# Kernel tuning notes

Hardware: AMD Instinct MI355X
Metric: run time of the kernel (lower is better)

## Reference

```python
import jax, jax.numpy as jnp
import numpy as np

B, S, D, H = 4, 2048, 1024, 16
HD = D // H  # head_size = 64


def setup_inputs() -> dict:
    key = jax.random.key(0)
    kx, kq, kk, kv = jax.random.split(key, 4)
    scale = 1.0 / np.sqrt(D)
    return {
        "x": jax.random.normal(kx, (B, S, D), dtype=jnp.float32),
        "Wq": jax.random.normal(kq, (H, HD, D), dtype=jnp.float32) * scale,
        "Wk": jax.random.normal(kk, (H, HD, D), dtype=jnp.float32) * scale,
        "Wv": jax.random.normal(kv, (H, HD, D), dtype=jnp.float32) * scale,
    }


def reference(x, Wq, Wk, Wv):
    # Per-head projections (Linear with weight [out, in]: y = x @ W.T),
    # vectorized over heads: [B,S,D] x [H,HD,D] -> [B,H,S,HD]
    q = jnp.einsum('bsd,hed->bhse', x, Wq)
    k = jnp.einsum('bsd,hed->bhse', x, Wk)
    v = jnp.einsum('bsd,hed->bhse', x, Wv)

    # Scaled scores: [B,H,S,S]
    att = jnp.einsum('bhqe,bhke->bhqk', q, k) / jnp.sqrt(jnp.asarray(HD, x.dtype))

    # Causal mask (lower-triangular incl. diagonal)
    causal = jnp.tril(jnp.ones((S, S), dtype=bool))
    att = jnp.where(causal, att, -jnp.inf)
    att = jax.nn.softmax(att, axis=-1)

    # Weighted values, then concat heads along feature dim -> [B,S,D]
    out = jnp.einsum('bhqk,bhke->bhqe', att, v)
    out = out.transpose(0, 2, 1, 3).reshape(B, S, H * HD)
    return out
```

## Files before the change

kernel.cpp:

```cpp
#include <hip/hip_runtime.h>
#include <hip/hip_bf16.h>

#define BATCH 4
#define S_LEN 2048
#define D_DIM 1024
#define NHEAD 16
#define HDIM 64

#define QSCALE 0.18033688011112042f

typedef __attribute__((ext_vector_type(8))) __bf16 bf16x8;
typedef __attribute__((ext_vector_type(4))) __bf16 bf16x4;
typedef __attribute__((ext_vector_type(4))) float f32x4;

static __device__ inline unsigned int bf16_bits(float f) {
    __bf16 h = (__bf16)f;
    return (unsigned int)__builtin_bit_cast(unsigned short, h);
}

__global__ __launch_bounds__(256) void cvt_kernel(
    const float* __restrict__ src, __bf16* __restrict__ dst, int n8)
{
    int i = blockIdx.x * 256 + threadIdx.x;
    if (i >= n8) return;
    const f32x4* p = reinterpret_cast<const f32x4*>(src + (size_t)i * 8);
    f32x4 a = p[0], b = p[1];
    bf16x8 r;
    r[0] = (__bf16)a[0]; r[1] = (__bf16)a[1]; r[2] = (__bf16)a[2]; r[3] = (__bf16)a[3];
    r[4] = (__bf16)b[0]; r[5] = (__bf16)b[1]; r[6] = (__bf16)b[2]; r[7] = (__bf16)b[3];
    *reinterpret_cast<bf16x8*>(dst + (size_t)i * 8) = r;
}

__global__ __launch_bounds__(256) void proj_gemm_kernel(
    const __bf16* __restrict__ xb, const __bf16* __restrict__ wb,
    __bf16* __restrict__ qo, __bf16* __restrict__ ko, __bf16* __restrict__ vto)
{
    __shared__ __bf16 As[128][32];
    __shared__ __bf16 Bs[128][32];

    const int tid = threadIdx.x;
    const int l  = tid & 63;
    const int w  = tid >> 6;
    const int wm = w >> 1, wn = w & 1;
    const int lr = l & 15, lg = l >> 4, lk = lg * 8;
    const int m0 = blockIdx.y * 128;
    const int n0 = blockIdx.x * 128;
    const int mat = n0 >> 10;
    const int nb  = n0 & 1023;

    const int sr = l >> 2;
    const int sc = (l & 3) * 8;
    const int g0 = w * 2;

    f32x4 acc[4][4] = {};

    for (int d = 0; d < D_DIM; d += 32) {
        __builtin_amdgcn_global_load_lds(
            (const __attribute__((address_space(1))) void*)(xb + (size_t)(m0 + g0 * 16 + sr) * D_DIM + d + sc),
            (__attribute__((address_space(3))) void*)(&As[g0 * 16][0]), 16, 0, 0);
        __builtin_amdgcn_global_load_lds(
            (const __attribute__((address_space(1))) void*)(xb + (size_t)(m0 + (g0 + 1) * 16 + sr) * D_DIM + d + sc),
            (__attribute__((address_space(3))) void*)(&As[(g0 + 1) * 16][0]), 16, 0, 0);
        __builtin_amdgcn_global_load_lds(
            (const __attribute__((address_space(1))) void*)(wb + (size_t)(n0 + g0 * 16 + sr) * D_DIM + d + sc),
            (__attribute__((address_space(3))) void*)(&Bs[g0 * 16][0]), 16, 0, 0);
        __builtin_amdgcn_global_load_lds(
            (const __attribute__((address_space(1))) void*)(wb + (size_t)(n0 + (g0 + 1) * 16 + sr) * D_DIM + d + sc),
            (__attribute__((address_space(3))) void*)(&Bs[(g0 + 1) * 16][0]), 16, 0, 0);
        __syncthreads();

        bf16x8 af[4], bfr[4];
        #pragma unroll
        for (int mi = 0; mi < 4; ++mi)
            af[mi] = *reinterpret_cast<const bf16x8*>(&As[wm * 64 + mi * 16 + lr][lk]);
        #pragma unroll
        for (int ni = 0; ni < 4; ++ni)
            bfr[ni] = *reinterpret_cast<const bf16x8*>(&Bs[wn * 64 + ni * 16 + lr][lk]);
        #pragma unroll
        for (int mi = 0; mi < 4; ++mi) {
            #pragma unroll
            for (int ni = 0; ni < 4; ++ni)
                acc[mi][ni] = __builtin_amdgcn_mfma_f32_16x16x32_bf16(
                    af[mi], bfr[ni], acc[mi][ni], 0, 0, 0);
        }
        __syncthreads();
    }

    const float oscale = (mat == 0) ? QSCALE : 1.0f;
    #pragma unroll
    for (int mi = 0; mi < 4; ++mi) {
        const int mrow = m0 + wm * 64 + mi * 16 + lg * 4;
        const int b = mrow >> 11;
        const int s = mrow & (S_LEN - 1);
        #pragma unroll
        for (int ni = 0; ni < 4; ++ni) {
            const int n = nb + wn * 64 + ni * 16 + lr;
            const int h = n >> 6;
            const int e = n & 63;
            if (mat == 2) {
                bf16x4 pk;
                #pragma unroll
                for (int r = 0; r < 4; ++r) pk[r] = (__bf16)acc[mi][ni][r];
                *reinterpret_cast<bf16x4*>(
                    vto + ((size_t)(b * NHEAD + h) * HDIM + e) * S_LEN + s) = pk;
            } else {
                __bf16* __restrict__ dst = (mat == 0) ? qo : ko;
                #pragma unroll
                for (int r = 0; r < 4; ++r)
                    dst[((size_t)(b * NHEAD + h) * S_LEN + (s + r)) * HDIM + e] =
                        (__bf16)(acc[mi][ni][r] * oscale);
            }
        }
    }
}

template<bool MASK>
__device__ __attribute__((always_inline)) inline void quad_iter(
    int kv0, int qbase, int lr, int lg, int lk, int swz,
    const __bf16* __restrict__ kp, const __bf16* __restrict__ vp,
    const bf16x8 (&bq0)[4], const bf16x8 (&bq1)[4],
    float (&m_acc)[4], float (&l_acc)[4], f32x4 (&acc)[4][4],
    __bf16* pl_base)
{
    bf16x8 ka0[4], ka1[4];
    #pragma unroll
    for (int c = 0; c < 4; ++c) {
        const __bf16* krow = kp + (size_t)(kv0 + c * 16 + lr) * HDIM;
        ka0[c] = *reinterpret_cast<const bf16x8*>(krow + lk);
        ka1[c] = *reinterpret_cast<const bf16x8*>(krow + 32 + lk);
    }
    bf16x8 av[2][4];
    #pragma unroll
    for (int c2 = 0; c2 < 2; ++c2)
        #pragma unroll
        for (int ni = 0; ni < 4; ++ni)
            av[c2][ni] = *reinterpret_cast<const bf16x8*>(
                vp + (size_t)(ni * 16 + lr) * S_LEN + kv0 + c2 * 32 + lk);

    #pragma unroll
    for (int i = 0; i < 4; ++i) {
        __bf16* pl = pl_base + i * (16 * 64);
        f32x4 s[4];
        __builtin_amdgcn_s_setprio(1);
        #pragma unroll
        for (int c = 0; c < 4; ++c) {
            f32x4 tt = {};
            tt = __builtin_amdgcn_mfma_f32_16x16x32_bf16(ka0[c], bq0[i], tt, 0, 0, 0);
            tt = __builtin_amdgcn_mfma_f32_16x16x32_bf16(ka1[c], bq1[i], tt, 0, 0, 0);
            s[c] = tt;
        }
        __builtin_amdgcn_s_setprio(0);

        if (MASK) {
            const int qrow = qbase + i * 16 + lr;
            #pragma unroll
            for (int c = 0; c < 4; ++c)
                #pragma unroll
                for (int r = 0; r < 4; ++r)
                    if (kv0 + c * 16 + lg * 4 + r > qrow) s[c][r] = -1e30f;
        }

        float a0 = fmaxf(fmaxf(s[0][0], s[0][1]), fmaxf(s[0][2], s[0][3]));
        float a1 = fmaxf(fmaxf(s[1][0], s[1][1]), fmaxf(s[1][2], s[1][3]));
        float a2 = fmaxf(fmaxf(s[2][0], s[2][1]), fmaxf(s[2][2], s[2][3]));
        float a3 = fmaxf(fmaxf(s[3][0], s[3][1]), fmaxf(s[3][2], s[3][3]));
        float mx = fmaxf(fmaxf(a0, a1), fmaxf(a2, a3));
        mx = fmaxf(mx, __shfl_xor(mx, 16));
        mx = fmaxf(mx, __shfl_xor(mx, 32));

        const float mnew = fmaxf(m_acc[i], mx);
        const float sc = exp2f(m_acc[i] - mnew);
        m_acc[i] = mnew;

        float psum = 0.0f;
        #pragma unroll
        for (int c = 0; c < 4; ++c) {
            const float p0 = exp2f(s[c][0] - mnew);
            const float p1 = exp2f(s[c][1] - mnew);
            const float p2 = exp2f(s[c][2] - mnew);
            const float p3 = exp2f(s[c][3] - mnew);
            psum += (p0 + p1) + (p2 + p3);
            uint2 pk;
            pk.x = bf16_bits(p0) | (bf16_bits(p1) << 16);
            pk.y = bf16_bits(p2) | (bf16_bits(p3) << 16);
            *reinterpret_cast<uint2*>(pl + lr * 64 + ((c * 16 + lg * 4) ^ swz)) = pk;
        }
        psum += __shfl_xor(psum, 16);
        psum += __shfl_xor(psum, 32);
        l_acc[i] = l_acc[i] * sc + psum;

        #pragma unroll
        for (int ni = 0; ni < 4; ++ni) acc[i][ni] *= sc;
    }

    __builtin_amdgcn_s_setprio(1);
    #pragma unroll
    for (int c2 = 0; c2 < 2; ++c2) {
        #pragma unroll
        for (int i = 0; i < 4; ++i) {
            __bf16* pl = pl_base + i * (16 * 64);
            const bf16x8 pa = *reinterpret_cast<const bf16x8*>(
                pl + lr * 64 + ((c2 * 32 + lk) ^ swz));
            #pragma unroll
            for (int ni = 0; ni < 4; ++ni)
                acc[i][ni] = __builtin_amdgcn_mfma_f32_16x16x32_bf16(
                    av[c2][ni], pa, acc[i][ni], 0, 0, 0);
        }
    }
    __builtin_amdgcn_s_setprio(0);
}

__global__ __launch_bounds__(64, 2) void attn_kernel(
    const __bf16* __restrict__ q, const __bf16* __restrict__ k,
    const __bf16* __restrict__ vt, float* __restrict__ out)
{
    __shared__ __bf16 plds[4][16][64];

    const int l  = threadIdx.x;
    const int lr = l & 15;
    const int lg = l >> 4;
    const int lk = lg * 8;
    const int swz = (lr & 7) << 3;

    const int n   = blockIdx.x;
    const int xcd = n & 7;
    const int m   = n >> 3;
    const int qq  = 31 - (m >> 3);
    const int bh  = xcd * 8 + (m & 7);

    const __bf16* __restrict__ kp = k  + (size_t)bh * S_LEN * HDIM;
    const __bf16* __restrict__ vp = vt + (size_t)bh * HDIM * S_LEN;
    const int bq = bh >> 4;
    const int hq = bh & 15;

    const int qbase = qq * 64;
    const int iters = qq + 1;

    const __bf16* __restrict__ qp = q + ((size_t)bh * S_LEN + qbase) * HDIM;
    bf16x8 bq0[4], bq1[4];
    #pragma unroll
    for (int i = 0; i < 4; ++i) {
        bq0[i] = *reinterpret_cast<const bf16x8*>(qp + (size_t)(i * 16 + lr) * HDIM + lk);
        bq1[i] = *reinterpret_cast<const bf16x8*>(qp + (size_t)(i * 16 + lr) * HDIM + 32 + lk);
    }

    float m_acc[4], l_acc[4];
    f32x4 acc[4][4] = {};
    #pragma unroll
    for (int i = 0; i < 4; ++i) { m_acc[i] = -1e30f; l_acc[i] = 0.0f; }

    __bf16* pl_base = &plds[0][0][0];

    #pragma unroll 1
    for (int j = 0; j < iters - 1; ++j)
        quad_iter<false>(j * 64, qbase, lr, lg, lk, swz, kp, vp,
                         bq0, bq1, m_acc, l_acc, acc, pl_base);
    quad_iter<true>((iters - 1) * 64, qbase, lr, lg, lk, swz, kp, vp,
                    bq0, bq1, m_acc, l_acc, acc, pl_base);

    #pragma unroll
    for (int i = 0; i < 4; ++i) {
        const float liv = 1.0f / l_acc[i];
        float* orow = out + (size_t)(bq * S_LEN + qbase + i * 16 + lr) * D_DIM + hq * HDIM;
        #pragma unroll
        for (int ni = 0; ni < 4; ++ni) {
            f32x4 ox;
            #pragma unroll
            for (int r = 0; r < 4; ++r) ox[r] = acc[i][ni][r] * liv;
            *reinterpret_cast<f32x4*>(orow + ni * 16 + lg * 4) = ox;
        }
    }
}

extern "C" void kernel_launch(void* const* d_in, const int* in_sizes, int n_in,
                              void* d_out, int out_size, void* d_ws, size_t ws_size,
                              hipStream_t stream)
{
    const float* x  = (const float*)d_in[0];
    const float* Wq = (const float*)d_in[1];
    const float* Wk = (const float*)d_in[2];
    const float* Wv = (const float*)d_in[3];
    float* out = (float*)d_out;

    const size_t x_elems = (size_t)BATCH * S_LEN * D_DIM;
    const size_t w_elems = (size_t)D_DIM * D_DIM;
    __bf16* xb   = (__bf16*)d_out;
    __bf16* wcat = xb + x_elems;

    const size_t per_buf = (size_t)BATCH * NHEAD * S_LEN * HDIM;
    __bf16* qb = (__bf16*)d_ws;
    __bf16* kb = qb + per_buf;
    __bf16* vb = kb + per_buf;

    cvt_kernel<<<(int)(x_elems / 8 / 256), 256, 0, stream>>>(x, xb, (int)(x_elems / 8));
    cvt_kernel<<<(int)(w_elems / 8 / 256), 256, 0, stream>>>(Wq, wcat, (int)(w_elems / 8));
    cvt_kernel<<<(int)(w_elems / 8 / 256), 256, 0, stream>>>(Wk, wcat + w_elems, (int)(w_elems / 8));
    cvt_kernel<<<(int)(w_elems / 8 / 256), 256, 0, stream>>>(Wv, wcat + 2 * w_elems, (int)(w_elems / 8));

    dim3 grid1(3 * D_DIM / 128, (BATCH * S_LEN) / 128);
    proj_gemm_kernel<<<grid1, dim3(256), 0, stream>>>(xb, wcat, qb, kb, vb);

    attn_kernel<<<dim3(2048), dim3(64), 0, stream>>>(qb, kb, vb, out);
}
```

Baseline: 193.0 us.

## Double-buffer K fragments across KV tiles and interleave softmax of row pairs

Adds register double-buffering of K fragments: the next KV tile's K is prefetched from global memory while the current tile is computed, using two KFrag sets and a ping-pong flag. It also processes two 16-row query sub-blocks at a time so their MFMA chains, reductions and shuffles interleave, and defers the l_acc cross-lane sum until after the PV MFMAs. V loads are reordered so the two halves of each row are fetched together. The extra live registers for the second K buffer raise pressure under launch_bounds(64,2) and may cause spills.

```diff
diff --git a/kernel.cpp b/kernel.cpp
--- a/kernel.cpp
+++ b/kernel.cpp
@@ -114,100 +114,149 @@
     }
 }
 
+struct KFrag { bf16x8 a0[4]; bf16x8 a1[4]; };
+struct VFrag { bf16x8 v0[4]; bf16x8 v1[4]; };
+
+__device__ __attribute__((always_inline)) inline void load_k(
+    KFrag& kf, const __bf16* __restrict__ kp, int kv0, int lr, int lk)
+{
+    #pragma unroll
+    for (int c = 0; c < 4; ++c) {
+        const __bf16* krow = kp + (size_t)(kv0 + c * 16 + lr) * HDIM;
+        kf.a0[c] = *reinterpret_cast<const bf16x8*>(krow + lk);
+        kf.a1[c] = *reinterpret_cast<const bf16x8*>(krow + 32 + lk);
+    }
+}
+
 template<bool MASK>
-__device__ __attribute__((always_inline)) inline void quad_iter(
+__device__ __attribute__((always_inline)) inline void quad_compute(
     int kv0, int qbase, int lr, int lg, int lk, int swz,
-    const __bf16* __restrict__ kp, const __bf16* __restrict__ vp,
+    const __bf16* __restrict__ vp, const KFrag& kf,
     const bf16x8 (&bq0)[4], const bf16x8 (&bq1)[4],
     float (&m_acc)[4], float (&l_acc)[4], f32x4 (&acc)[4][4],
     __bf16* pl_base)
 {
-    bf16x8 ka0[4], ka1[4];
-    #pragma unroll
-    for (int c = 0; c < 4; ++c) {
-        const __bf16* krow = kp + (size_t)(kv0 + c * 16 + lr) * HDIM;
-        ka0[c] = *reinterpret_cast<const bf16x8*>(krow + lk);
-        ka1[c] = *reinterpret_cast<const bf16x8*>(krow + 32 + lk);
-    }
-    bf16x8 av[2][4];
-    #pragma unroll
-    for (int c2 = 0; c2 < 2; ++c2)
-        #pragma unroll
-        for (int ni = 0; ni < 4; ++ni)
-            av[c2][ni] = *reinterpret_cast<const bf16x8*>(
-                vp + (size_t)(ni * 16 + lr) * S_LEN + kv0 + c2 * 32 + lk);
-
-    #pragma unroll
-    for (int i = 0; i < 4; ++i) {
-        __bf16* pl = pl_base + i * (16 * 64);
-        f32x4 s[4];
+    VFrag vf;
+    #pragma unroll
+    for (int ni = 0; ni < 4; ++ni) {
+        const __bf16* vrow = vp + (size_t)(ni * 16 + lr) * S_LEN + kv0;
+        vf.v0[ni] = *reinterpret_cast<const bf16x8*>(vrow + lk);
+        vf.v1[ni] = *reinterpret_cast<const bf16x8*>(vrow + 32 + lk);
+    }
+
+    float sc_t[4], psum_t[4];
+
+    #pragma unroll
+    for (int pp = 0; pp < 2; ++pp) {
+        const int i0 = pp * 2, i1 = pp * 2 + 1;
+        f32x4 sA[4], sB[4];
+
         __builtin_amdgcn_s_setprio(1);
         #pragma unroll
         for (int c = 0; c < 4; ++c) {
-            f32x4 tt = {};
-            tt = __builtin_amdgcn_mfma_f32_16x16x32_bf16(ka0[c], bq0[i], tt, 0, 0, 0);
-            tt = __builtin_amdgcn_mfma_f32_16x16x32_bf16(ka1[c], bq1[i], tt, 0, 0, 0);
-            s[c] = tt;
+            f32x4 t0 = {}, t1 = {};
+            t0 = __builtin_amdgcn_mfma_f32_16x16x32_bf16(kf.a0[c], bq0[i0], t0, 0, 0, 0);
+            t0 = __builtin_amdgcn_mfma_f32_16x16x32_bf16(kf.a1[c], bq1[i0], t0, 0, 0, 0);
+            t1 = __builtin_amdgcn_mfma_f32_16x16x32_bf16(kf.a0[c], bq0[i1], t1, 0, 0, 0);
+            t1 = __builtin_amdgcn_mfma_f32_16x16x32_bf16(kf.a1[c], bq1[i1], t1, 0, 0, 0);
+            sA[c] = t0; sB[c] = t1;
         }
         __builtin_amdgcn_s_setprio(0);
 
         if (MASK) {
-            const int qrow = qbase + i * 16 + lr;
+            const int qrA = qbase + i0 * 16 + lr;
+            const int qrB = qbase + i1 * 16 + lr;
             #pragma unroll
             for (int c = 0; c < 4; ++c)
                 #pragma unroll
-                for (int r = 0; r < 4; ++r)
-                    if (kv0 + c * 16 + lg * 4 + r > qrow) s[c][r] = -1e30f;
-        }
-
-        float a0 = fmaxf(fmaxf(s[0][0], s[0][1]), fmaxf(s[0][2], s[0][3]));
-        float a1 = fmaxf(fmaxf(s[1][0], s[1][1]), fmaxf(s[1][2], s[1][3]));
-        float a2 = fmaxf(fmaxf(s[2][0], s[2][1]), fmaxf(s[2][2], s[2][3]));
-        float a3 = fmaxf(fmaxf(s[3][0], s[3][1]), fmaxf(s[3][2], s[3][3]));
-        float mx = fmaxf(fmaxf(a0, a1), fmaxf(a2, a3));
-        mx = fmaxf(mx, __shfl_xor(mx, 16));
-        mx = fmaxf(mx, __shfl_xor(mx, 32));
-
-        const float mnew = fmaxf(m_acc[i], mx);
-        const float sc = exp2f(m_acc[i] - mnew);
-        m_acc[i] = mnew;
-
-        float psum = 0.0f;
+                for (int r = 0; r < 4; ++r) {
+                    const int kvp = kv0 + c * 16 + lg * 4 + r;
+                    if (kvp > qrA) sA[c][r] = -1e30f;
+                    if (kvp > qrB) sB[c][r] = -1e30f;
+                }
+        }
+
+        float mxA = fmaxf(
+            fmaxf(fmaxf(fmaxf(sA[0][0], sA[0][1]), fmaxf(sA[0][2], sA[0][3])),
+                  fmaxf(fmaxf(sA[1][0], sA[1][1]), fmaxf(sA[1][2], sA[1][3]))),
+            fmaxf(fmaxf(fmaxf(sA[2][0], sA[2][1]), fmaxf(sA[2][2], sA[2][3])),
+                  fmaxf(fmaxf(sA[3][0], sA[3][1]), fmaxf(sA[3][2], sA[3][3]))));
+        float mxB = fmaxf(
+            fmaxf(fmaxf(fmaxf(sB[0][0], sB[0][1]), fmaxf(sB[0][2], sB[0][3])),
+                  fmaxf(fmaxf(sB[1][0], sB[1][1]), fmaxf(sB[1][2], sB[1][3]))),
+            fmaxf(fmaxf(fmaxf(sB[2][0], sB[2][1]), fmaxf(sB[2][2], sB[2][3])),
+                  fmaxf(fmaxf(sB[3][0], sB[3][1]), fmaxf(sB[3][2], sB[3][3]))));
+        float tA = __shfl_xor(mxA, 16);
+        float tB = __shfl_xor(mxB, 16);
+        mxA = fmaxf(mxA, tA);
+        mxB = fmaxf(mxB, tB);
+        tA = __shfl_xor(mxA, 32);
+        tB = __shfl_xor(mxB, 32);
+        mxA = fmaxf(mxA, tA);
+        mxB = fmaxf(mxB, tB);
+
+        const float mnA = fmaxf(m_acc[i0], mxA);
+        const float mnB = fmaxf(m_acc[i1], mxB);
+        sc_t[i0] = exp2f(m_acc[i0] - mnA);
+        sc_t[i1] = exp2f(m_acc[i1] - mnB);
+        m_acc[i0] = mnA;
+        m_acc[i1] = mnB;
+
+        __bf16* plA = pl_base + i0 * (16 * 64);
+        __bf16* plB = pl_base + i1 * (16 * 64);
+        float psA = 0.0f, psB = 0.0f;
         #pragma unroll
         for (int c = 0; c < 4; ++c) {
-            const float p0 = exp2f(s[c][0] - mnew);
-            const float p1 = exp2f(s[c][1] - mnew);
-            const float p2 = exp2f(s[c][2] - mnew);
-            const float p3 = exp2f(s[c][3] - mnew);
-            psum += (p0 + p1) + (p2 + p3);
-            uint2 pk;
-            pk.x = bf16_bits(p0) | (bf16_bits(p1) << 16);
-            pk.y = bf16_bits(p2) | (bf16_bits(p3) << 16);
-            *reinterpret_cast<uint2*>(pl + lr * 64 + ((c * 16 + lg * 4) ^ swz)) = pk;
-        }
-        psum += __shfl_xor(psum, 16);
-        psum += __shfl_xor(psum, 32);
-        l_acc[i] = l_acc[i] * sc + psum;
-
-        #pragma unroll
-        for (int ni = 0; ni < 4; ++ni) acc[i][ni] *= sc;
+            const float a0 = exp2f(sA[c][0] - mnA);
+            const float a1 = exp2f(sA[c][1] - mnA);
+            const float a2 = exp2f(sA[c][2] - mnA);
+            const float a3 = exp2f(sA[c][3] - mnA);
+            const float b0 = exp2f(sB[c][0] - mnB);
+            const float b1 = exp2f(sB[c][1] - mnB);
+            const float b2 = exp2f(sB[c][2] - mnB);
+            const float b3 = exp2f(sB[c][3] - mnB);
+            psA += (a0 + a1) + (a2 + a3);
+            psB += (b0 + b1) + (b2 + b3);
+            uint2 pkA, pkB;
+            pkA.x = bf16_bits(a0) | (bf16_bits(a1) << 16);
+            pkA.y = bf16_bits(a2) | (bf16_bits(a3) << 16);
+            pkB.x = bf16_bits(b0) | (bf16_bits(b1) << 16);
+            pkB.y = bf16_bits(b2) | (bf16_bits(b3) << 16);
+            const int col = (c * 16 + lg * 4) ^ swz;
+            *reinterpret_cast<uint2*>(plA + lr * 64 + col) = pkA;
+            *reinterpret_cast<uint2*>(plB + lr * 64 + col) = pkB;
+        }
+        psum_t[i0] = psA;
+        psum_t[i1] = psB;
+
+        #pragma unroll
+        for (int ni = 0; ni < 4; ++ni) {
+            acc[i0][ni] *= sc_t[i0];
+            acc[i1][ni] *= sc_t[i1];
+        }
     }
 
     __builtin_amdgcn_s_setprio(1);
     #pragma unroll
-    for (int c2 = 0; c2 < 2; ++c2) {
-        #pragma unroll
-        for (int i = 0; i < 4; ++i) {
-            __bf16* pl = pl_base + i * (16 * 64);
-            const bf16x8 pa = *reinterpret_cast<const bf16x8*>(
-                pl + lr * 64 + ((c2 * 32 + lk) ^ swz));
-            #pragma unroll
-            for (int ni = 0; ni < 4; ++ni)
-                acc[i][ni] = __builtin_amdgcn_mfma_f32_16x16x32_bf16(
-                    av[c2][ni], pa, acc[i][ni], 0, 0, 0);
+    for (int i = 0; i < 4; ++i) {
+        __bf16* pl = pl_base + i * (16 * 64);
+        const bf16x8 pa0 = *reinterpret_cast<const bf16x8*>(pl + lr * 64 + ((0 + lk) ^ swz));
+        const bf16x8 pa1 = *reinterpret_cast<const bf16x8*>(pl + lr * 64 + ((32 + lk) ^ swz));
+        #pragma unroll
+        for (int ni = 0; ni < 4; ++ni) {
+            acc[i][ni] = __builtin_amdgcn_mfma_f32_16x16x32_bf16(vf.v0[ni], pa0, acc[i][ni], 0, 0, 0);
+            acc[i][ni] = __builtin_amdgcn_mfma_f32_16x16x32_bf16(vf.v1[ni], pa1, acc[i][ni], 0, 0, 0);
         }
     }
     __builtin_amdgcn_s_setprio(0);
+
+    #pragma unroll
+    for (int i = 0; i < 4; ++i) {
+        float ps = psum_t[i];
+        ps += __shfl_xor(ps, 16);
+        ps += __shfl_xor(ps, 32);
+        l_acc[i] = l_acc[i] * sc_t[i] + ps;
+    }
 }
 
 __global__ __launch_bounds__(64, 2) void attn_kernel(
@@ -251,12 +300,29 @@
 
     __bf16* pl_base = &plds[0][0][0];
 
+    KFrag kA, kB;
+    load_k(kA, kp, 0, lr, lk);
+    bool useA = true;
+
     #pragma unroll 1
-    for (int j = 0; j < iters - 1; ++j)
-        quad_iter<false>(j * 64, qbase, lr, lg, lk, swz, kp, vp,
-                         bq0, bq1, m_acc, l_acc, acc, pl_base);
-    quad_iter<true>((iters - 1) * 64, qbase, lr, lg, lk, swz, kp, vp,
-                    bq0, bq1, m_acc, l_acc, acc, pl_base);
+    for (int j = 0; j < iters - 1; ++j) {
+        if (useA) {
+            load_k(kB, kp, (j + 1) * 64, lr, lk);
+            quad_compute<false>(j * 64, qbase, lr, lg, lk, swz, vp, kA,
+                                bq0, bq1, m_acc, l_acc, acc, pl_base);
+        } else {
+            load_k(kA, kp, (j + 1) * 64, lr, lk);
+            quad_compute<false>(j * 64, qbase, lr, lg, lk, swz, vp, kB,
+                                bq0, bq1, m_acc, l_acc, acc, pl_base);
+        }
+        useA = !useA;
+    }
+    if (useA)
+        quad_compute<true>((iters - 1) * 64, qbase, lr, lg, lk, swz, vp, kA,
+                           bq0, bq1, m_acc, l_acc, acc, pl_base);
+    else
+        quad_compute<true>((iters - 1) * 64, qbase, lr, lg, lk, swz, vp, kB,
+                           bq0, bq1, m_acc, l_acc, acc, pl_base);
 
     #pragma unroll
     for (int i = 0; i < 4; ++i) {
```

Result: slower. 355.8 us (+84.3%).

## Double-buffer K tiles in LDS via async global_load_lds prefetch

Applied to the files above, without the earlier changes.

K tiles now go into a double-buffered LDS region with asynchronous global-to-LDS loads. The next tile is prefetched while the current one is computed, and the K operand is read back from LDS with an XOR swizzle. This is meant to hide global-memory latency for K behind the MFMA and softmax work. The cost is extra LDS use, which can affect occupancy, and manual vmcnt waits. Those waits also count the V global loads, so the vmcnt(8) threshold may not line up with the intended K dependency.

```diff
diff --git a/kernel.cpp b/kernel.cpp
--- a/kernel.cpp
+++ b/kernel.cpp
@@ -114,28 +114,39 @@
     }
 }
 
+__device__ __attribute__((always_inline)) inline void stage_k(
+    __bf16* kbuf, const __bf16* __restrict__ kp, int kv0, int l)
+{
+    const int rsub = l >> 3;
+    const int csw  = ((l & 7) ^ rsub) << 3;
+    #pragma unroll
+    for (int ch = 0; ch < 8; ++ch) {
+        __builtin_amdgcn_global_load_lds(
+            (const __attribute__((address_space(1))) void*)(
+                kp + (size_t)(kv0 + ch * 8 + rsub) * HDIM + csw),
+            (__attribute__((address_space(3))) void*)(kbuf + ch * 512),
+            16, 0, 0);
+    }
+}
+
 template<bool MASK>
-__device__ __attribute__((always_inline)) inline void quad_iter(
+__device__ __attribute__((always_inline)) inline void quad_compute(
     int kv0, int qbase, int lr, int lg, int lk, int swz,
-    const __bf16* __restrict__ kp, const __bf16* __restrict__ vp,
+    const __bf16* __restrict__ vp, const __bf16* __restrict__ kb,
     const bf16x8 (&bq0)[4], const bf16x8 (&bq1)[4],
     float (&m_acc)[4], float (&l_acc)[4], f32x4 (&acc)[4][4],
     __bf16* pl_base)
 {
-    bf16x8 ka0[4], ka1[4];
-    #pragma unroll
-    for (int c = 0; c < 4; ++c) {
-        const __bf16* krow = kp + (size_t)(kv0 + c * 16 + lr) * HDIM;
-        ka0[c] = *reinterpret_cast<const bf16x8*>(krow + lk);
-        ka1[c] = *reinterpret_cast<const bf16x8*>(krow + 32 + lk);
-    }
+    const int kcol0 = (lg * 8) ^ ((lr & 7) << 3);
+    const int kcol1 = (32 + lg * 8) ^ ((lr & 7) << 3);
+
     bf16x8 av[2][4];
     #pragma unroll
-    for (int c2 = 0; c2 < 2; ++c2)
-        #pragma unroll
-        for (int ni = 0; ni < 4; ++ni)
-            av[c2][ni] = *reinterpret_cast<const bf16x8*>(
-                vp + (size_t)(ni * 16 + lr) * S_LEN + kv0 + c2 * 32 + lk);
+    for (int ni = 0; ni < 4; ++ni) {
+        const __bf16* vrow = vp + (size_t)(ni * 16 + lr) * S_LEN + kv0;
+        av[0][ni] = *reinterpret_cast<const bf16x8*>(vrow + lk);
+        av[1][ni] = *reinterpret_cast<const bf16x8*>(vrow + 32 + lk);
+    }
 
     #pragma unroll
     for (int i = 0; i < 4; ++i) {
@@ -144,9 +155,12 @@
         __builtin_amdgcn_s_setprio(1);
         #pragma unroll
         for (int c = 0; c < 4; ++c) {
+            const int row = c * 16 + lr;
+            const bf16x8 ka0 = *reinterpret_cast<const bf16x8*>(kb + row * 64 + kcol0);
+            const bf16x8 ka1 = *reinterpret_cast<const bf16x8*>(kb + row * 64 + kcol1);
             f32x4 tt = {};
-            tt = __builtin_amdgcn_mfma_f32_16x16x32_bf16(ka0[c], bq0[i], tt, 0, 0, 0);
-            tt = __builtin_amdgcn_mfma_f32_16x16x32_bf16(ka1[c], bq1[i], tt, 0, 0, 0);
+            tt = __builtin_amdgcn_mfma_f32_16x16x32_bf16(ka0, bq0[i], tt, 0, 0, 0);
+            tt = __builtin_amdgcn_mfma_f32_16x16x32_bf16(ka1, bq1[i], tt, 0, 0, 0);
             s[c] = tt;
         }
         __builtin_amdgcn_s_setprio(0);
@@ -215,6 +229,7 @@
     const __bf16* __restrict__ vt, float* __restrict__ out)
 {
     __shared__ __bf16 plds[4][16][64];
+    __shared__ __bf16 klds[2][64 * 64];
 
     const int l  = threadIdx.x;
     const int lr = l & 15;
@@ -251,12 +266,25 @@
 
     __bf16* pl_base = &plds[0][0][0];
 
+    stage_k(&klds[0][0], kp, 0, l);
+    asm volatile("s_waitcnt vmcnt(0)" ::: "memory");
+    __builtin_amdgcn_sched_barrier(0);
+
     #pragma unroll 1
-    for (int j = 0; j < iters - 1; ++j)
-        quad_iter<false>(j * 64, qbase, lr, lg, lk, swz, kp, vp,
-                         bq0, bq1, m_acc, l_acc, acc, pl_base);
-    quad_iter<true>((iters - 1) * 64, qbase, lr, lg, lk, swz, kp, vp,
-                    bq0, bq1, m_acc, l_acc, acc, pl_base);
+    for (int j = 0; j < iters - 1; ++j) {
+        stage_k(&klds[(j & 1) ^ 1][0], kp, (j + 1) * 64, l);
+        __builtin_amdgcn_sched_barrier(0);
+        asm volatile("s_waitcnt vmcnt(8)" ::: "memory");
+        __builtin_amdgcn_sched_barrier(0);
+        quad_compute<false>(j * 64, qbase, lr, lg, lk, swz, vp, &klds[j & 1][0],
+                            bq0, bq1, m_acc, l_acc, acc, pl_base);
+    }
+    __builtin_amdgcn_sched_barrier(0);
+    asm volatile("s_waitcnt vmcnt(0)" ::: "memory");
+    __builtin_amdgcn_sched_barrier(0);
+    quad_compute<true>((iters - 1) * 64, qbase, lr, lg, lk, swz, vp,
+                       &klds[(iters - 1) & 1][0],
+                       bq0, bq1, m_acc, l_acc, acc, pl_base);
 
     #pragma unroll
     for (int i = 0; i < 4; ++i) {
```

New measurement: 197.5 us. 2.3% more time.

## Split attention KV loop across two waves and merge partial softmax results

Applied to the files above, without the earlier changes.

Each attention block now runs two wavefronts that take alternating 64-wide KV tiles for the same 64 query rows. Each wave keeps its own running max, sum and accumulator. At the end the partial states are exchanged through shared memory and merged with a rescaled online-softmax combine. The aim is to halve the serial KV loop length per block and improve latency hiding, at the cost of extra LDS traffic, two barriers, and duplicated Q register loads per wave.

```diff
diff --git a/kernel.cpp b/kernel.cpp
--- a/kernel.cpp
+++ b/kernel.cpp
@@ -115,7 +115,7 @@
 }
 
 template<bool MASK>
-__device__ __attribute__((always_inline)) inline void quad_iter(
+__device__ __attribute__((always_inline)) inline void quad_compute(
     int kv0, int qbase, int lr, int lg, int lk, int swz,
     const __bf16* __restrict__ kp, const __bf16* __restrict__ vp,
     const bf16x8 (&bq0)[4], const bf16x8 (&bq1)[4],
@@ -131,11 +131,11 @@
     }
     bf16x8 av[2][4];
     #pragma unroll
-    for (int c2 = 0; c2 < 2; ++c2)
-        #pragma unroll
-        for (int ni = 0; ni < 4; ++ni)
-            av[c2][ni] = *reinterpret_cast<const bf16x8*>(
-                vp + (size_t)(ni * 16 + lr) * S_LEN + kv0 + c2 * 32 + lk);
+    for (int ni = 0; ni < 4; ++ni) {
+        const __bf16* vrow = vp + (size_t)(ni * 16 + lr) * S_LEN + kv0;
+        av[0][ni] = *reinterpret_cast<const bf16x8*>(vrow + lk);
+        av[1][ni] = *reinterpret_cast<const bf16x8*>(vrow + 32 + lk);
+    }
 
     #pragma unroll
     for (int i = 0; i < 4; ++i) {
@@ -210,13 +210,15 @@
     __builtin_amdgcn_s_setprio(0);
 }
 
-__global__ __launch_bounds__(64, 2) void attn_kernel(
+__global__ __launch_bounds__(128, 3) void attn_kernel(
     const __bf16* __restrict__ q, const __bf16* __restrict__ k,
     const __bf16* __restrict__ vt, float* __restrict__ out)
 {
-    __shared__ __bf16 plds[4][16][64];
-
-    const int l  = threadIdx.x;
+    __shared__ __align__(16) unsigned char smem[16384 + 512];
+
+    const int tid = threadIdx.x;
+    const int l  = tid & 63;
+    const int w  = tid >> 6;
     const int lr = l & 15;
     const int lg = l >> 4;
     const int lk = lg * 8;
@@ -234,7 +236,6 @@
     const int hq = bh & 15;
 
     const int qbase = qq * 64;
-    const int iters = qq + 1;
 
     const __bf16* __restrict__ qp = q + ((size_t)bh * S_LEN + qbase) * HDIM;
     bf16x8 bq0[4], bq1[4];
@@ -249,24 +250,53 @@
     #pragma unroll
     for (int i = 0; i < 4; ++i) { m_acc[i] = -1e30f; l_acc[i] = 0.0f; }
 
-    __bf16* pl_base = &plds[0][0][0];
+    __bf16* pl_base = reinterpret_cast<__bf16*>(smem) + w * 4096;
 
     #pragma unroll 1
-    for (int j = 0; j < iters - 1; ++j)
-        quad_iter<false>(j * 64, qbase, lr, lg, lk, swz, kp, vp,
-                         bq0, bq1, m_acc, l_acc, acc, pl_base);
-    quad_iter<true>((iters - 1) * 64, qbase, lr, lg, lk, swz, kp, vp,
-                    bq0, bq1, m_acc, l_acc, acc, pl_base);
-
-    #pragma unroll
-    for (int i = 0; i < 4; ++i) {
-        const float liv = 1.0f / l_acc[i];
-        float* orow = out + (size_t)(bq * S_LEN + qbase + i * 16 + lr) * D_DIM + hq * HDIM;
+    for (int j = w; j < qq; j += 2)
+        quad_compute<false>(j * 64, qbase, lr, lg, lk, swz, kp, vp,
+                            bq0, bq1, m_acc, l_acc, acc, pl_base);
+    if ((qq & 1) == w)
+        quad_compute<true>(qq * 64, qbase, lr, lg, lk, swz, kp, vp,
+                           bq0, bq1, m_acc, l_acc, acc, pl_base);
+
+    float* accbuf = reinterpret_cast<float*>(smem);
+    float* mbuf   = reinterpret_cast<float*>(smem + 16384);
+    float* lbuf   = mbuf + 64;
+
+    __syncthreads();
+    #pragma unroll
+    for (int tt = 0; tt < 2; ++tt) {
+        const int t = 2 * w + tt;
+        #pragma unroll
+        for (int ni = 0; ni < 4; ++ni)
+            #pragma unroll
+            for (int r = 0; r < 4; ++r)
+                accbuf[t * 1024 + (ni * 16 + lg * 4 + r) * 16 + lr] = acc[t][ni][r];
+        if (lg == 0) {
+            mbuf[t * 16 + lr] = m_acc[t];
+            lbuf[t * 16 + lr] = l_acc[t];
+        }
+    }
+    __syncthreads();
+    #pragma unroll
+    for (int tt = 0; tt < 2; ++tt) {
+        const int t = 2 * (1 - w) + tt;
+        const float mo = mbuf[t * 16 + lr];
+        const float lo = lbuf[t * 16 + lr];
+        const float mn = fmaxf(m_acc[t], mo);
+        const float s_own = exp2f(m_acc[t] - mn);
+        const float s_oth = exp2f(mo - mn);
+        const float liv = 1.0f / (l_acc[t] * s_own + lo * s_oth);
+        float* orow = out + (size_t)(bq * S_LEN + qbase + t * 16 + lr) * D_DIM + hq * HDIM;
         #pragma unroll
         for (int ni = 0; ni < 4; ++ni) {
             f32x4 ox;
             #pragma unroll
-            for (int r = 0; r < 4; ++r) ox[r] = acc[i][ni][r] * liv;
+            for (int r = 0; r < 4; ++r) {
+                const float oth = accbuf[t * 1024 + (ni * 16 + lg * 4 + r) * 16 + lr];
+                ox[r] = (acc[t][ni][r] * s_own + oth * s_oth) * liv;
+            }
             *reinterpret_cast<f32x4*>(orow + ni * 16 + lg * 4) = ox;
         }
     }
@@ -300,5 +330,5 @@
     dim3 grid1(3 * D_DIM / 128, (BATCH * S_LEN) / 128);
     proj_gemm_kernel<<<grid1, dim3(256), 0, stream>>>(xb, wcat, qb, kb, vb);
 
-    attn_kernel<<<dim3(2048), dim3(64), 0, stream>>>(qb, kb, vb, out);
-}
+    attn_kernel<<<dim3(2048), dim3(128), 0, stream>>>(qb, kb, vb, out);
+}
```

New measurement: 317.2 us. 64.4% more time.
